# Kernel tuning notes

Hardware: AMD Instinct MI355X
Metric: run time of the kernel (lower is better)

Reference implementation:

```python
import jax, jax.numpy as jnp
import numpy as np

N_NODES = 50000


def _gcn_conv(x, src, dst, deg_inv_sqrt, W, b, n_nodes):
    # PyG GCNConv: linear transform, then symmetric-normalized aggregation.
    xw = x @ W  # [N, out_dim]
    norm = deg_inv_sqrt[src] * deg_inv_sqrt[dst]  # [E]
    msg = xw[src] * norm[:, None]  # [E, out_dim] gathered messages
    out = jax.ops.segment_sum(msg, dst, num_segments=n_nodes)
    return out + b


def setup_inputs() -> dict:
    key = jax.random.key(0)
    ks = jax.random.split(key, 10)
    n, d_in, d_h, d_z = N_NODES, 128, 128, 64
    e = 800000
    x = jax.random.normal(ks[0], (n, d_in), dtype=jnp.float32)
    edge_index = jax.random.randint(ks[1], (2, e), 0, n, dtype=jnp.int64)
    eps = jax.random.normal(ks[2], (n, d_z), dtype=jnp.float32)
    s_in = 1.0 / np.sqrt(d_in)
    s_h = 1.0 / np.sqrt(d_h)
    W1 = jax.random.normal(ks[3], (d_in, d_h), dtype=jnp.float32) * s_in
    b1 = jnp.zeros((d_h,), dtype=jnp.float32)
    Wmu = jax.random.normal(ks[4], (d_h, d_z), dtype=jnp.float32) * s_h
    bmu = jnp.zeros((d_z,), dtype=jnp.float32)
    Wls = jax.random.normal(ks[5], (d_h, d_z), dtype=jnp.float32) * s_h
    bls = jnp.zeros((d_z,), dtype=jnp.float32)
    return {"x": x, "edge_index": edge_index, "eps": eps,
            "W1": W1, "b1": b1, "Wmu": Wmu, "bmu": bmu, "Wls": Wls, "bls": bls}


def reference(x, edge_index, eps, W1, b1, Wmu, bmu, Wls, bls):
    n = x.shape[0]
    loops = jnp.arange(n, dtype=edge_index.dtype)
    src = jnp.concatenate([edge_index[0], loops])  # add self-loops
    dst = jnp.concatenate([edge_index[1], loops])
    deg = jax.ops.segment_sum(jnp.ones_like(dst, dtype=x.dtype), dst, num_segments=n)
    deg_inv_sqrt = jnp.where(deg > 0, jax.lax.rsqrt(deg), 0.0)

    hidden = jax.nn.relu(_gcn_conv(x, src, dst, deg_inv_sqrt, W1, b1, n))
    mu = _gcn_conv(hidden, src, dst, deg_inv_sqrt, Wmu, bmu, n)
    logstd = _gcn_conv(hidden, src, dst, deg_inv_sqrt, Wls, bls, n)
    z = mu + eps * jnp.exp(logstd)  # reparameterize (training mode)
    return (z, mu, logstd)
```

## Files before the change

### kernel.cpp

```cpp
#include <hip/hip_runtime.h>
#include <math.h>

#define LDP 136
#define EPB 4096

typedef short v8s __attribute__((ext_vector_type(8)));
typedef float f32x4 __attribute__((ext_vector_type(4)));

static __device__ __forceinline__ unsigned short f2bf(float f) {
    unsigned u = __builtin_bit_cast(unsigned, f);
    return (unsigned short)((u + 0x7FFFu + ((u >> 16) & 1u)) >> 16);
}
static __device__ __forceinline__ float bf_lo(unsigned u) {
    return __builtin_bit_cast(float, u << 16);
}
static __device__ __forceinline__ float bf_hi(unsigned u) {
    return __builtin_bit_cast(float, u & 0xFFFF0000u);
}


__global__ __launch_bounds__(256) void coarse_hist(const int* __restrict__ dst,
                                                   int* __restrict__ ccnt, int e, int nb) {
    __shared__ int h[256];
    int t = threadIdx.x;
    h[t] = 0;
    __syncthreads();
    for (int i = blockIdx.x * 256 + t; i < e; i += gridDim.x * 256)
        atomicAdd(&h[dst[i] >> 8], 1);
    __syncthreads();
    if (t < nb && h[t]) atomicAdd(&ccnt[t], h[t]);
}

__global__ __launch_bounds__(256) void coarse_scan(const int* __restrict__ ccnt,
                                                   int* __restrict__ coffs,
                                                   int* __restrict__ ccur, int nb) {
    __shared__ int buf[256];
    int t = threadIdx.x;
    int v = (t < nb) ? ccnt[t] : 0;
    buf[t] = v;
    __syncthreads();
    for (int off = 1; off < 256; off <<= 1) {
        int add = (t >= off) ? buf[t - off] : 0;
        __syncthreads();
        buf[t] += add;
        __syncthreads();
    }
    int excl = buf[t] - v;
    if (t < nb) { coffs[t] = excl; ccur[t] = excl; }
    if (t == nb - 1) coffs[nb] = buf[t];
}

__global__ __launch_bounds__(256) void part_edges(const int* __restrict__ src,
                                                  const int* __restrict__ dst,
                                                  int* __restrict__ ccur,
                                                  unsigned* __restrict__ pak, int e, int nb) {
    __shared__ int h[256];
    __shared__ int cur[256];
    int t = threadIdx.x;
    h[t] = 0;
    __syncthreads();
    int beg = blockIdx.x * EPB;
    int end = min(e, beg + EPB);
    for (int i = beg + t; i < end; i += 256)
        atomicAdd(&h[dst[i] >> 8], 1);
    __syncthreads();
    if (t < nb) {
        int c = h[t];
        cur[t] = c ? atomicAdd(&ccur[t], c) : 0;
    }
    __syncthreads();
    for (int i = beg + t; i < end; i += 256) {
        int d = dst[i];
        int pos = atomicAdd(&cur[d >> 8], 1);
        pak[pos] = (unsigned)src[i] | ((unsigned)(d & 255) << 16);
    }
}

__global__ __launch_bounds__(256) void build_csr(const unsigned* __restrict__ pak,
                                                 const int* __restrict__ coffs,
                                                 int* __restrict__ offs,
                                                 float* __restrict__ dis,
                                                 unsigned short* __restrict__ csr, int n) {
    __shared__ int cnt[256];
    __shared__ int buf[256];
    __shared__ int cur[256];
    int t = threadIdx.x;
    int b = blockIdx.x;
    int ebeg = coffs[b], eend = coffs[b + 1];
    cnt[t] = 0;
    __syncthreads();
    for (int i = ebeg + t; i < eend; i += 256)
        atomicAdd(&cnt[pak[i] >> 16], 1);
    __syncthreads();
    int v = cnt[t];
    buf[t] = v;
    __syncthreads();
    for (int off = 1; off < 256; off <<= 1) {
        int add = (t >= off) ? buf[t - off] : 0;
        __syncthreads();
        buf[t] += add;
        __syncthreads();
    }
    int start = ebeg + buf[t] - v;
    cur[t] = start;
    int node = (b << 8) + t;
    if (node < n) {
        offs[node] = start + v;
        dis[node] = rsqrtf(1.0f + (float)v);
    }
    __syncthreads();
    for (int i = ebeg + t; i < eend; i += 256) {
        unsigned p = pak[i];
        int pos = atomicAdd(&cur[p >> 16], 1);
        csr[pos] = (unsigned short)(p & 0xFFFFu);
    }
}

__global__ void prep_w(const float* __restrict__ W1, const float* __restrict__ Wmu,
                       const float* __restrict__ Wls,
                       unsigned short* __restrict__ WT1, unsigned short* __restrict__ WTc) {
    int i = blockIdx.x * 256 + threadIdx.x;
    if (i < 16384) {
        int j = i >> 7, k = i & 127;
        WT1[i] = f2bf(W1[k * 128 + j]);
    } else if (i < 32768) {
        int i2 = i - 16384;
        int j = i2 >> 7, k = i2 & 127;
        WTc[i2] = f2bf(j < 64 ? Wmu[k * 64 + j] : Wls[k * 64 + (j - 64)]);
    }
}

__global__ __launch_bounds__(256) void gemm1(const float* __restrict__ x,
                                             const unsigned short* __restrict__ WT,
                                             const float* __restrict__ dis,
                                             unsigned short* __restrict__ XWb, int n) {
    __shared__ unsigned short Wt[128 * LDP];
    int t = threadIdx.x;
    {
        const unsigned* Wg = (const unsigned*)WT;
        unsigned* Wl = (unsigned*)Wt;
        for (int i = t; i < 128 * 64; i += 256) {
            int j = i >> 6, k2 = i & 63;
            Wl[j * (LDP / 2) + k2] = Wg[i];
        }
    }
    int lane = t & 63, ww = t >> 6;
    int l15 = lane & 15, quad = lane >> 4;
    int base = blockIdx.x * 64;
    int arow = base + ww * 16 + l15;
    v8s afr[4];
    if (arow < n) {
        const float4* xr = (const float4*)(x + (long)arow * 128);
        #pragma unroll
        for (int kk = 0; kk < 4; ++kk) {
            float4 f0 = xr[kk * 8 + quad * 2];
            float4 f1 = xr[kk * 8 + quad * 2 + 1];
            uint4 p;
            p.x = (unsigned)f2bf(f0.x) | ((unsigned)f2bf(f0.y) << 16);
            p.y = (unsigned)f2bf(f0.z) | ((unsigned)f2bf(f0.w) << 16);
            p.z = (unsigned)f2bf(f1.x) | ((unsigned)f2bf(f1.y) << 16);
            p.w = (unsigned)f2bf(f1.z) | ((unsigned)f2bf(f1.w) << 16);
            afr[kk] = __builtin_bit_cast(v8s, p);
        }
    } else {
        uint4 z = make_uint4(0, 0, 0, 0);
        #pragma unroll
        for (int kk = 0; kk < 4; ++kk) afr[kk] = __builtin_bit_cast(v8s, z);
    }
    __syncthreads();
    f32x4 acc[8];
    #pragma unroll
    for (int i = 0; i < 8; ++i) acc[i] = (f32x4){0.f, 0.f, 0.f, 0.f};
    #pragma unroll
    for (int tt = 0; tt < 8; ++tt) {
        const unsigned short* Brow = Wt + (tt * 16 + l15) * LDP;
        #pragma unroll
        for (int kk = 0; kk < 4; ++kk) {
            uint4 u = *(const uint4*)(Brow + kk * 32 + quad * 8);
            v8s bfr = __builtin_bit_cast(v8s, u);
            acc[tt] = __builtin_amdgcn_mfma_f32_16x16x32_bf16(afr[kk], bfr, acc[tt], 0, 0, 0);
        }
    }
    #pragma unroll
    for (int reg = 0; reg < 4; ++reg) {
        int row = base + ww * 16 + quad * 4 + reg;
        if (row >= n) continue;
        float d = dis[row];
        unsigned short* orow = XWb + (long)row * 128;
        #pragma unroll
        for (int tt = 0; tt < 8; ++tt)
            orow[tt * 16 + l15] = f2bf(acc[tt][reg] * d);
    }
}

__global__ __launch_bounds__(256) void gather128(const unsigned* __restrict__ inb,
                                                 const int* __restrict__ offs,
                                                 const unsigned short* __restrict__ csr,
                                                 const float* __restrict__ dis,
                                                 const float* __restrict__ bias,
                                                 unsigned* __restrict__ outb,
                                                 int n, int mode) {
    int lane = threadIdx.x & 63;
    int i = blockIdx.x * 4 + (threadIdx.x >> 6);
    if (i >= n) return;
    int end = offs[i];
    int beg = (i == 0) ? 0 : offs[i - 1];
    float di = dis[i];
    unsigned su = inb[(long)i * 64 + lane];
    float a0 = bf_lo(su), a1 = bf_hi(su);
    float b0 = 0.f, b1 = 0.f, c0 = 0.f, c1 = 0.f, d0 = 0.f, d1 = 0.f;
    for (int cbeg = beg; cbeg < end; cbeg += 64) {
        int cc = end - cbeg; if (cc > 64) cc = 64;
        int myidx = (lane < cc) ? (int)csr[cbeg + lane] : 0;
        int jj = 0;
        for (; jj + 3 < cc; jj += 4) {
            int sA = __shfl(myidx, jj);
            int sB = __shfl(myidx, jj + 1);
            int sC = __shfl(myidx, jj + 2);
            int sD = __shfl(myidx, jj + 3);
            unsigned uA = inb[(long)sA * 64 + lane];
            unsigned uB = inb[(long)sB * 64 + lane];
            unsigned uC = inb[(long)sC * 64 + lane];
            unsigned uD = inb[(long)sD * 64 + lane];
            a0 += bf_lo(uA); a1 += bf_hi(uA);
            b0 += bf_lo(uB); b1 += bf_hi(uB);
            c0 += bf_lo(uC); c1 += bf_hi(uC);
            d0 += bf_lo(uD); d1 += bf_hi(uD);
        }
        for (; jj < cc; ++jj) {
            int sA = __shfl(myidx, jj);
            unsigned uA = inb[(long)sA * 64 + lane];
            a0 += bf_lo(uA); a1 += bf_hi(uA);
        }
    }
    float r0 = di * ((a0 + b0) + (c0 + d0));
    float r1 = di * ((a1 + b1) + (c1 + d1));
    if (mode) {
        r0 += bias[lane * 2];     r0 = fmaxf(r0, 0.f) * di;
        r1 += bias[lane * 2 + 1]; r1 = fmaxf(r1, 0.f) * di;
    }
    outb[(long)i * 64 + lane] = (unsigned)f2bf(r0) | ((unsigned)f2bf(r1) << 16);
}

__global__ __launch_bounds__(256) void epi(const unsigned* __restrict__ AGGb,
                                           const unsigned short* __restrict__ WTc,
                                           const float* __restrict__ bmu,
                                           const float* __restrict__ bls,
                                           const float* __restrict__ eps,
                                           float* Zo, float* MUo, float* LSo, int n) {
    __shared__ unsigned short Wt[128 * LDP];
    int t = threadIdx.x;
    {
        const unsigned* Wg = (const unsigned*)WTc;
        unsigned* Wl = (unsigned*)Wt;
        for (int i = t; i < 128 * 64; i += 256) {
            int j = i >> 6, k2 = i & 63;
            Wl[j * (LDP / 2) + k2] = Wg[i];
        }
    }
    int lane = t & 63, ww = t >> 6;
    int l15 = lane & 15, quad = lane >> 4;
    int base = blockIdx.x * 64;
    int arow = base + ww * 16 + l15;
    v8s afr[4];
    if (arow < n) {
        const uint4* ar = (const uint4*)(AGGb + (long)arow * 64);
        #pragma unroll
        for (int kk = 0; kk < 4; ++kk)
            afr[kk] = __builtin_bit_cast(v8s, ar[kk * 4 + quad]);
    } else {
        uint4 z = make_uint4(0, 0, 0, 0);
        #pragma unroll
        for (int kk = 0; kk < 4; ++kk) afr[kk] = __builtin_bit_cast(v8s, z);
    }
    __syncthreads();
    f32x4 acc[8];
    #pragma unroll
    for (int i = 0; i < 8; ++i) acc[i] = (f32x4){0.f, 0.f, 0.f, 0.f};
    #pragma unroll
    for (int tt = 0; tt < 8; ++tt) {
        const unsigned short* Brow = Wt + (tt * 16 + l15) * LDP;
        #pragma unroll
        for (int kk = 0; kk < 4; ++kk) {
            uint4 u = *(const uint4*)(Brow + kk * 32 + quad * 8);
            v8s bfr = __builtin_bit_cast(v8s, u);
            acc[tt] = __builtin_amdgcn_mfma_f32_16x16x32_bf16(afr[kk], bfr, acc[tt], 0, 0, 0);
        }
    }
    #pragma unroll
    for (int reg = 0; reg < 4; ++reg) {
        int row = base + ww * 16 + quad * 4 + reg;
        if (row >= n) continue;
        #pragma unroll
        for (int tt = 0; tt < 4; ++tt) {
            int c = tt * 16 + l15;
            long o = (long)row * 64 + c;
            float m = acc[tt][reg] + bmu[c];
            float l = acc[tt + 4][reg] + bls[c];
            Zo[o]  = m + eps[o] * __expf(l);
            MUo[o] = m;
            LSo[o] = l;
        }
    }
}

extern "C" void kernel_launch(void* const* d_in, const int* in_sizes, int n_in,
                              void* d_out, int out_size, void* d_ws, size_t ws_size,
                              hipStream_t stream) {
    const float* x   = (const float*)d_in[0];
    const int*   ei  = (const int*)d_in[1];
    const float* eps = (const float*)d_in[2];
    const float* W1  = (const float*)d_in[3];
    const float* b1  = (const float*)d_in[4];
    const float* Wmu = (const float*)d_in[5];
    const float* bmu = (const float*)d_in[6];
    const float* Wls = (const float*)d_in[7];
    const float* bls = (const float*)d_in[8];

    int n = in_sizes[0] / 128;
    int e = in_sizes[1] / 2;
    const int* src = ei;
    const int* dst = ei + e;
    long nh = (long)n * 64;
    int P = (n + 255) & ~255;
    int NB = (n + 255) >> 8;

    float*          dis   = (float*)d_ws;
    int*            offs  = (int*)(dis + P);
    unsigned short* csr16 = (unsigned short*)(offs + P);
    unsigned short* WT1   = csr16 + ((e + 1) & ~1);
    unsigned short* WTc   = WT1 + 16384;
    int*            ccnt  = (int*)(WTc + 16384);
    int*            coffs = ccnt + 256;
    int*            ccur  = coffs + 258;

    float* A = (float*)d_out;
    float* B = A + nh;
    float* C = A + 2 * nh;
    unsigned short* XWb  = (unsigned short*)C;
    unsigned*       Hb   = (unsigned*)A;
    unsigned*       AGGb = (unsigned*)B;
    unsigned*       pak  = (unsigned*)A;

    int gb  = (n + 63) / 64;
    int gbn = (n + 3) / 4;
    int pb  = (e + EPB - 1) / EPB;

    hipMemsetAsync(ccnt, 0, (size_t)NB * sizeof(int), stream);
    prep_w<<<128, 256, 0, stream>>>(W1, Wmu, Wls, WT1, WTc);
    coarse_hist<<<pb, 256, 0, stream>>>(dst, ccnt, e, NB);
    coarse_scan<<<1, 256, 0, stream>>>(ccnt, coffs, ccur, NB);
    part_edges<<<pb, 256, 0, stream>>>(src, dst, ccur, pak, e, NB);
    build_csr<<<NB, 256, 0, stream>>>(pak, coffs, offs, dis, csr16, n);

    gemm1<<<gb, 256, 0, stream>>>(x, WT1, dis, XWb, n);

    gather128<<<gbn, 256, 0, stream>>>((const unsigned*)XWb, offs, csr16, dis, b1, Hb, n, 1);

    gather128<<<gbn, 256, 0, stream>>>(Hb, offs, csr16, dis, b1, AGGb, n, 0);

    epi<<<gb, 256, 0, stream>>>(AGGb, WTc, bmu, bls, eps, A, B, C, n);
}
```

Baseline: 230.8 us.

## Split feature matrix into 32-column slices for cache-resident gathers

```diff
diff --git a/kernel.cpp b/kernel.cpp
--- a/kernel.cpp
+++ b/kernel.cpp
@@ -186,60 +186,71 @@
         int row = base + ww * 16 + quad * 4 + reg;
         if (row >= n) continue;
         float d = dis[row];
-        unsigned short* orow = XWb + (long)row * 128;
-        #pragma unroll
-        for (int tt = 0; tt < 8; ++tt)
-            orow[tt * 16 + l15] = f2bf(acc[tt][reg] * d);
-    }
-}
-
-__global__ __launch_bounds__(256) void gather128(const unsigned* __restrict__ inb,
-                                                 const int* __restrict__ offs,
-                                                 const unsigned short* __restrict__ csr,
-                                                 const float* __restrict__ dis,
-                                                 const float* __restrict__ bias,
-                                                 unsigned* __restrict__ outb,
-                                                 int n, int mode) {
-    int lane = threadIdx.x & 63;
-    int i = blockIdx.x * 4 + (threadIdx.x >> 6);
+        #pragma unroll
+        for (int tt = 0; tt < 8; ++tt) {
+            long off = (long)(tt >> 1) * n * 32 + (long)row * 32 + (tt & 1) * 16 + l15;
+            XWb[off] = f2bf(acc[tt][reg] * d);
+        }
+    }
+}
+
+__global__ __launch_bounds__(256) void gather32(const unsigned short* __restrict__ in_sl,
+                                                const int* __restrict__ offs,
+                                                const unsigned short* __restrict__ csr,
+                                                const float* __restrict__ dis,
+                                                const float* __restrict__ bias,
+                                                unsigned short* __restrict__ out,
+                                                long out_rs, long out_ss,
+                                                int n, int bps, int mode) {
+    int t = threadIdx.x;
+    int lane = t & 63;
+    int s = blockIdx.x / bps;
+    int i = (blockIdx.x - s * bps) * 4 + (t >> 6);
     if (i >= n) return;
+    int q = lane & 7, o = lane >> 3;
+    const unsigned short* sl = in_sl + (long)s * n * 32;
     int end = offs[i];
     int beg = (i == 0) ? 0 : offs[i - 1];
     float di = dis[i];
-    unsigned su = inb[(long)i * 64 + lane];
-    float a0 = bf_lo(su), a1 = bf_hi(su);
-    float b0 = 0.f, b1 = 0.f, c0 = 0.f, c1 = 0.f, d0 = 0.f, d1 = 0.f;
+    float a0 = 0.f, a1 = 0.f, a2 = 0.f, a3 = 0.f;
+    if (o == 0) {
+        uint2 u = *(const uint2*)(sl + (long)i * 32 + q * 4);
+        a0 = bf_lo(u.x); a1 = bf_hi(u.x); a2 = bf_lo(u.y); a3 = bf_hi(u.y);
+    }
     for (int cbeg = beg; cbeg < end; cbeg += 64) {
         int cc = end - cbeg; if (cc > 64) cc = 64;
         int myidx = (lane < cc) ? (int)csr[cbeg + lane] : 0;
-        int jj = 0;
-        for (; jj + 3 < cc; jj += 4) {
-            int sA = __shfl(myidx, jj);
-            int sB = __shfl(myidx, jj + 1);
-            int sC = __shfl(myidx, jj + 2);
-            int sD = __shfl(myidx, jj + 3);
-            unsigned uA = inb[(long)sA * 64 + lane];
-            unsigned uB = inb[(long)sB * 64 + lane];
-            unsigned uC = inb[(long)sC * 64 + lane];
-            unsigned uD = inb[(long)sD * 64 + lane];
-            a0 += bf_lo(uA); a1 += bf_hi(uA);
-            b0 += bf_lo(uB); b1 += bf_hi(uB);
-            c0 += bf_lo(uC); c1 += bf_hi(uC);
-            d0 += bf_lo(uD); d1 += bf_hi(uD);
-        }
-        for (; jj < cc; ++jj) {
-            int sA = __shfl(myidx, jj);
-            unsigned uA = inb[(long)sA * 64 + lane];
-            a0 += bf_lo(uA); a1 += bf_hi(uA);
-        }
-    }
-    float r0 = di * ((a0 + b0) + (c0 + d0));
-    float r1 = di * ((a1 + b1) + (c1 + d1));
-    if (mode) {
-        r0 += bias[lane * 2];     r0 = fmaxf(r0, 0.f) * di;
-        r1 += bias[lane * 2 + 1]; r1 = fmaxf(r1, 0.f) * di;
-    }
-    outb[(long)i * 64 + lane] = (unsigned)f2bf(r0) | ((unsigned)f2bf(r1) << 16);
+        for (int jj = 0; jj < cc; jj += 8) {
+            int sj = __shfl(myidx, jj + o);
+            if (jj + o < cc) {
+                uint2 u = *(const uint2*)(sl + (long)sj * 32 + q * 4);
+                a0 += bf_lo(u.x); a1 += bf_hi(u.x);
+                a2 += bf_lo(u.y); a3 += bf_hi(u.y);
+            }
+        }
+    }
+    #pragma unroll
+    for (int d = 8; d < 64; d <<= 1) {
+        a0 += __shfl_xor(a0, d);
+        a1 += __shfl_xor(a1, d);
+        a2 += __shfl_xor(a2, d);
+        a3 += __shfl_xor(a3, d);
+    }
+    if (o == 0) {
+        float r0, r1, r2, r3;
+        if (mode) {
+            float4 b4 = ((const float4*)bias)[s * 8 + q];
+            r0 = fmaxf(di * a0 + b4.x, 0.f) * di;
+            r1 = fmaxf(di * a1 + b4.y, 0.f) * di;
+            r2 = fmaxf(di * a2 + b4.z, 0.f) * di;
+            r3 = fmaxf(di * a3 + b4.w, 0.f) * di;
+        } else {
+            r0 = di * a0; r1 = di * a1; r2 = di * a2; r3 = di * a3;
+        }
+        unsigned lo = (unsigned)f2bf(r0) | ((unsigned)f2bf(r1) << 16);
+        unsigned hi = (unsigned)f2bf(r2) | ((unsigned)f2bf(r3) << 16);
+        *(uint2*)(out + (long)i * out_rs + (long)s * out_ss + q * 4) = make_uint2(lo, hi);
+    }
 }
 
 __global__ __launch_bounds__(256) void epi(const unsigned* __restrict__ AGGb,
@@ -338,12 +349,12 @@
     float* B = A + nh;
     float* C = A + 2 * nh;
     unsigned short* XWb  = (unsigned short*)C;
-    unsigned*       Hb   = (unsigned*)A;
-    unsigned*       AGGb = (unsigned*)B;
+    unsigned short* Hb   = (unsigned short*)A;
+    unsigned short* AGGb = (unsigned short*)B;
     unsigned*       pak  = (unsigned*)A;
 
     int gb  = (n + 63) / 64;
-    int gbn = (n + 3) / 4;
+    int bps = (n + 3) / 4;
     int pb  = (e + EPB - 1) / EPB;
 
     hipMemsetAsync(ccnt, 0, (size_t)NB * sizeof(int), stream);
@@ -355,9 +366,11 @@
 
     gemm1<<<gb, 256, 0, stream>>>(x, WT1, dis, XWb, n);
 
-    gather128<<<gbn, 256, 0, stream>>>((const unsigned*)XWb, offs, csr16, dis, b1, Hb, n, 1);
-
-    gather128<<<gbn, 256, 0, stream>>>(Hb, offs, csr16, dis, b1, AGGb, n, 0);
-
-    epi<<<gb, 256, 0, stream>>>(AGGb, WTc, bmu, bls, eps, A, B, C, n);
-}
+    gather32<<<4 * bps, 256, 0, stream>>>(XWb, offs, csr16, dis, b1, Hb,
+                                          32L, (long)n * 32, n, bps, 1);
+
+    gather32<<<4 * bps, 256, 0, stream>>>(Hb, offs, csr16, dis, b1, AGGb,
+                                          128L, 32L, n, bps, 0);
+
+    epi<<<gb, 256, 0, stream>>>((const unsigned*)AGGb, WTc, bmu, bls, eps, A, B, C, n);
+}
```

Result: slower. 309.9 us (+34.3%).

## Split gather into feature slices with 16 edges per wave in parallel

Applied to the files above, without the earlier changes.

```diff
diff --git a/kernel.cpp b/kernel.cpp
--- a/kernel.cpp
+++ b/kernel.cpp
@@ -193,53 +193,87 @@
     }
 }
 
-__global__ __launch_bounds__(256) void gather128(const unsigned* __restrict__ inb,
-                                                 const int* __restrict__ offs,
-                                                 const unsigned short* __restrict__ csr,
-                                                 const float* __restrict__ dis,
-                                                 const float* __restrict__ bias,
-                                                 unsigned* __restrict__ outb,
-                                                 int n, int mode) {
+__global__ __launch_bounds__(256) void gather_slice(const unsigned* __restrict__ inb,
+                                                    const int* __restrict__ offs,
+                                                    const unsigned short* __restrict__ csr,
+                                                    const float* __restrict__ dis,
+                                                    const float* __restrict__ bias,
+                                                    unsigned* __restrict__ outb,
+                                                    int n, int mode) {
+    int s = blockIdx.x & 3;
+    int nblk = blockIdx.x >> 2;
     int lane = threadIdx.x & 63;
-    int i = blockIdx.x * 4 + (threadIdx.x >> 6);
-    if (i >= n) return;
-    int end = offs[i];
-    int beg = (i == 0) ? 0 : offs[i - 1];
-    float di = dis[i];
-    unsigned su = inb[(long)i * 64 + lane];
-    float a0 = bf_lo(su), a1 = bf_hi(su);
-    float b0 = 0.f, b1 = 0.f, c0 = 0.f, c1 = 0.f, d0 = 0.f, d1 = 0.f;
-    for (int cbeg = beg; cbeg < end; cbeg += 64) {
-        int cc = end - cbeg; if (cc > 64) cc = 64;
-        int myidx = (lane < cc) ? (int)csr[cbeg + lane] : 0;
-        int jj = 0;
-        for (; jj + 3 < cc; jj += 4) {
-            int sA = __shfl(myidx, jj);
-            int sB = __shfl(myidx, jj + 1);
-            int sC = __shfl(myidx, jj + 2);
-            int sD = __shfl(myidx, jj + 3);
-            unsigned uA = inb[(long)sA * 64 + lane];
-            unsigned uB = inb[(long)sB * 64 + lane];
-            unsigned uC = inb[(long)sC * 64 + lane];
-            unsigned uD = inb[(long)sD * 64 + lane];
-            a0 += bf_lo(uA); a1 += bf_hi(uA);
-            b0 += bf_lo(uB); b1 += bf_hi(uB);
-            c0 += bf_lo(uC); c1 += bf_hi(uC);
-            d0 += bf_lo(uD); d1 += bf_hi(uD);
-        }
-        for (; jj < cc; ++jj) {
-            int sA = __shfl(myidx, jj);
-            unsigned uA = inb[(long)sA * 64 + lane];
-            a0 += bf_lo(uA); a1 += bf_hi(uA);
-        }
-    }
-    float r0 = di * ((a0 + b0) + (c0 + d0));
-    float r1 = di * ((a1 + b1) + (c1 + d1));
-    if (mode) {
-        r0 += bias[lane * 2];     r0 = fmaxf(r0, 0.f) * di;
-        r1 += bias[lane * 2 + 1]; r1 = fmaxf(r1, 0.f) * di;
-    }
-    outb[(long)i * 64 + lane] = (unsigned)f2bf(r0) | ((unsigned)f2bf(r1) << 16);
+    int w = threadIdx.x >> 6;
+    int qt = lane >> 2, b4 = lane & 3;
+    const unsigned* base = inb + s * 16 + b4 * 4;
+
+    for (int k = 0; k < 4; ++k) {
+        int i = nblk * 16 + w * 4 + k;
+        if (i >= n) break;
+        int end = offs[i];
+        int beg = (i == 0) ? 0 : offs[i - 1];
+        float di = dis[i];
+
+        float a0 = 0.f, a1 = 0.f, a2 = 0.f, a3 = 0.f;
+        float a4 = 0.f, a5 = 0.f, a6 = 0.f, a7 = 0.f;
+
+        if (qt == 0) {
+            uint4 u = *(const uint4*)(base + (long)i * 64);
+            a0 += bf_lo(u.x); a1 += bf_hi(u.x);
+            a2 += bf_lo(u.y); a3 += bf_hi(u.y);
+            a4 += bf_lo(u.z); a5 += bf_hi(u.z);
+            a6 += bf_lo(u.w); a7 += bf_hi(u.w);
+        }
+
+        for (int cbeg = beg; cbeg < end; cbeg += 64) {
+            int cc = end - cbeg; if (cc > 64) cc = 64;
+            int myidx = (lane < cc) ? (int)csr[cbeg + lane] : 0;
+            for (int g = 0; g < cc; g += 16) {
+                int eidx = g + qt;
+                int sg = __shfl(myidx, eidx);
+                if (eidx < cc) {
+                    uint4 u = *(const uint4*)(base + (long)sg * 64);
+                    a0 += bf_lo(u.x); a1 += bf_hi(u.x);
+                    a2 += bf_lo(u.y); a3 += bf_hi(u.y);
+                    a4 += bf_lo(u.z); a5 += bf_hi(u.z);
+                    a6 += bf_lo(u.w); a7 += bf_hi(u.w);
+                }
+            }
+        }
+
+        #pragma unroll
+        for (int d = 4; d < 64; d <<= 1) {
+            a0 += __shfl_xor(a0, d); a1 += __shfl_xor(a1, d);
+            a2 += __shfl_xor(a2, d); a3 += __shfl_xor(a3, d);
+            a4 += __shfl_xor(a4, d); a5 += __shfl_xor(a5, d);
+            a6 += __shfl_xor(a6, d); a7 += __shfl_xor(a7, d);
+        }
+
+        if (qt == 0) {
+            float r0, r1, r2, r3, r4, r5, r6, r7;
+            if (mode) {
+                const float4* bp = (const float4*)(bias + s * 32 + b4 * 8);
+                float4 bA = bp[0], bB = bp[1];
+                r0 = fmaxf(di * a0 + bA.x, 0.f) * di;
+                r1 = fmaxf(di * a1 + bA.y, 0.f) * di;
+                r2 = fmaxf(di * a2 + bA.z, 0.f) * di;
+                r3 = fmaxf(di * a3 + bA.w, 0.f) * di;
+                r4 = fmaxf(di * a4 + bB.x, 0.f) * di;
+                r5 = fmaxf(di * a5 + bB.y, 0.f) * di;
+                r6 = fmaxf(di * a6 + bB.z, 0.f) * di;
+                r7 = fmaxf(di * a7 + bB.w, 0.f) * di;
+            } else {
+                r0 = di * a0; r1 = di * a1; r2 = di * a2; r3 = di * a3;
+                r4 = di * a4; r5 = di * a5; r6 = di * a6; r7 = di * a7;
+            }
+            uint4 o;
+            o.x = (unsigned)f2bf(r0) | ((unsigned)f2bf(r1) << 16);
+            o.y = (unsigned)f2bf(r2) | ((unsigned)f2bf(r3) << 16);
+            o.z = (unsigned)f2bf(r4) | ((unsigned)f2bf(r5) << 16);
+            o.w = (unsigned)f2bf(r6) | ((unsigned)f2bf(r7) << 16);
+            *(uint4*)(outb + (long)i * 64 + s * 16 + b4 * 4) = o;
+        }
+    }
 }
 
 __global__ __launch_bounds__(256) void epi(const unsigned* __restrict__ AGGb,
@@ -343,7 +377,7 @@
     unsigned*       pak  = (unsigned*)A;
 
     int gb  = (n + 63) / 64;
-    int gbn = (n + 3) / 4;
+    int gsl = 4 * ((n + 15) / 16);
     int pb  = (e + EPB - 1) / EPB;
 
     hipMemsetAsync(ccnt, 0, (size_t)NB * sizeof(int), stream);
@@ -355,9 +389,9 @@
 
     gemm1<<<gb, 256, 0, stream>>>(x, WT1, dis, XWb, n);
 
-    gather128<<<gbn, 256, 0, stream>>>((const unsigned*)XWb, offs, csr16, dis, b1, Hb, n, 1);
-
-    gather128<<<gbn, 256, 0, stream>>>(Hb, offs, csr16, dis, b1, AGGb, n, 0);
+    gather_slice<<<gsl, 256, 0, stream>>>((const unsigned*)XWb, offs, csr16, dis, b1, Hb, n, 1);
+
+    gather_slice<<<gsl, 256, 0, stream>>>(Hb, offs, csr16, dis, b1, AGGb, n, 0);
 
     epi<<<gb, 256, 0, stream>>>(AGGb, WTc, bmu, bls, eps, A, B, C, n);
 }
```

New measurement: 322.3 us. +39.7%, slower.
